# Kernel tuning notes

Measured on AMD Instinct MI355X. Metric: run time of the kernel, lower is better.

## Reference

```python
import jax, jax.numpy as jnp
import numpy as np

B, N, IN_DIM, D, H, L = 8, 256, 2, 128, 512, 2
EPS = 1e-5


def layer_norm(x, g, b):
    m = jnp.mean(x, axis=-1, keepdims=True)
    v = jnp.var(x, axis=-1, keepdims=True)
    return (x - m) * jax.lax.rsqrt(v + EPS) * g + b


def loo_max_pool(nodes):
    # nodes: (B, N, D) -> leave-one-out max over the set axis -> (B, N, D)
    n = nodes.shape[1]
    neg = jnp.finfo(nodes.dtype).min
    mask = jnp.eye(n, dtype=bool)[None, :, :, None]          # (1, N, N, 1)
    expanded = jnp.broadcast_to(nodes[:, None, :, :],
                                (nodes.shape[0], n, n, nodes.shape[2]))
    return jnp.where(mask, neg, expanded).max(axis=2)        # (B, N, D)


def setup_inputs() -> dict:
    key = jax.random.key(0)
    ks = jax.random.split(key, 16)
    s = 0.02
    inp = {
        "x":   jax.random.normal(ks[0], (B, N, IN_DIM), dtype=jnp.float32),
        # embedding linear + its LayerNorm
        "We":  jax.random.normal(ks[1], (IN_DIM, D)) * s,
        "be":  jnp.zeros((D,), jnp.float32),
        "ge":  jnp.ones((D,), jnp.float32),
        "bge": jnp.zeros((D,), jnp.float32),
        # per-layer pool linear (concat of x and LOO-pooled context: 2D -> D)
        "Wp":  jax.random.normal(ks[2], (L, 2 * D, D)) * s,
        "bp":  jnp.zeros((L, D), jnp.float32),
        "gp":  jnp.ones((L, D), jnp.float32),
        "bgp": jnp.zeros((L, D), jnp.float32),
        # per-layer feed-forward D -> H -> D
        "W1":  jax.random.normal(ks[3], (L, D, H)) * s,
        "b1":  jnp.zeros((L, H), jnp.float32),
        "W2":  jax.random.normal(ks[4], (L, H, D)) * s,
        "b2":  jnp.zeros((L, D), jnp.float32),
        "gf":  jnp.ones((L, D), jnp.float32),
        "bgf": jnp.zeros((L, D), jnp.float32),
    }
    return inp


def reference(x, We, be, ge, bge, Wp, bp, gp, bgp, W1, b1, W2, b2, gf, bgf):
    # embeddings + embedding norm
    h = layer_norm(x @ We + be, ge, bge)                      # (B, N, D)
    for i in range(L):
        # pool layer: LOO max pooling, concat, linear, residual, norm
        pooled = loo_max_pool(h)                              # (B, N, D)
        cat = jnp.concatenate([h, pooled], axis=-1)           # (B, N, 2D)
        h = layer_norm(h + cat @ Wp[i] + bp[i], gp[i], bgp[i])
        # feed-forward, residual, norm
        ff = jax.nn.relu(h @ W1[i] + b1[i]) @ W2[i] + b2[i]
        h = layer_norm(h + ff, gf[i], bgf[i])
    return h
```

## Files before the change

### kernel.cpp

```cpp
#include <hip/hip_runtime.h>
#include <hip/hip_bf16.h>

#define BB 8
#define NN 256
#define DD 128
#define HH 512
#define LL 2
#define EPSV 1e-5f
#define TPE 4
#define TPB 8
#define BPE (NN/TPE)
#define BPL (NN/TPB)
#define NEMB ((BB*NN)/TPE)

typedef unsigned short ushort_t;
typedef __attribute__((ext_vector_type(8))) short bf16x8;
typedef __attribute__((ext_vector_type(4))) float f32x4;

__device__ __forceinline__ ushort_t f2b(float v){
  __hip_bfloat16 h = __float2bfloat16(v);
  return *(ushort_t*)&h;
}

__device__ __forceinline__ void waveRed2(float &a, float &b){
  #pragma unroll
  for (int off=32; off>=1; off>>=1){
    a += __shfl_xor(a, off, 64);
    b += __shfl_xor(b, off, 64);
  }
}

__device__ __forceinline__ void poolMerge(float &m1, float &m2, int &am,
                                          float o1, float o2, int oa){
  if (o1 > m1){ m2 = fmaxf(m1, o2); m1 = o1; am = oa; }
  else        { m2 = fmaxf(m2, o1); }
}

__global__ __launch_bounds__(512) void k_prep(
    const float* __restrict__ x, const float* __restrict__ We,
    const float* __restrict__ be, const float* __restrict__ ge,
    const float* __restrict__ bge, float* __restrict__ h,
    float* __restrict__ pm1p, float* __restrict__ pm2p, int* __restrict__ pargp,
    const float* __restrict__ Wp, const float* __restrict__ W1,
    const float* __restrict__ W2, ushort_t* __restrict__ wpT,
    ushort_t* __restrict__ w1T, ushort_t* __restrict__ w2T)
{
  __shared__ float tile[32][33];
  __shared__ float red[TPE][2][2];
  __shared__ float hf[TPE][DD];

  if (blockIdx.x < NEMB){
    int tid = threadIdx.x;
    int t = tid >> 7, d = tid & 127;
    int lane = tid & 63, wid = (tid >> 6) & 1;
    int t0 = blockIdx.x * TPE;
    int tok = t0 + t;
    float x0 = x[tok*2], x1 = x[tok*2+1];
    float v = fmaf(x0, We[d], fmaf(x1, We[DD+d], be[d]));
    float s=v, q=v*v; waveRed2(s,q);
    if (lane==0){ red[t][wid][0]=s; red[t][wid][1]=q; }
    __syncthreads();
    float S=red[t][0][0]+red[t][1][0], Q=red[t][0][1]+red[t][1][1];
    float m=S*(1.f/DD), var=Q*(1.f/DD)-m*m, rs=rsqrtf(var+EPSV);
    float hv = (v-m)*rs*ge[d] + bge[d];
    h[(size_t)tok*DD + d] = hv;
    hf[t][d] = hv;
    __syncthreads();
    if (t==0){
      int b = t0 >> 8;
      int n0 = t0 & 255;
      float m1 = hf[0][d], m2 = -3.4e38f; int am = n0;
      #pragma unroll
      for (int p=1;p<TPE;++p) poolMerge(m1,m2,am, hf[p][d], -3.4e38f, n0+p);
      int blk = (t0 >> 2) & (BPE-1);
      size_t idx = ((size_t)b*BPE + blk)*DD + d;
      pm1p[idx]=m1; pm2p[idx]=m2; pargp[idx]=am;
    }
  } else {
    if (threadIdx.x >= 256) return;
    int bid = blockIdx.x - NEMB;
    const float* src; ushort_t* dst; int K, N, kt, nt;
    if (bid < 64){
      int l = bid >> 5, r = bid & 31;
      src = Wp + (size_t)l*256*128; dst = wpT + (size_t)l*128*256;
      K=256; N=128; kt = r >> 2; nt = r & 3;
    } else if (bid < 192){
      int e = bid - 64; int l = e >> 6, r = e & 63;
      src = W1 + (size_t)l*128*512; dst = w1T + (size_t)l*512*128;
      K=128; N=512; kt = r >> 4; nt = r & 15;
    } else {
      int e = bid - 192; int l = e >> 6, r = e & 63;
      src = W2 + (size_t)l*512*128; dst = w2T + (size_t)l*128*512;
      K=512; N=128; kt = r >> 2; nt = r & 3;
    }
    int k0 = kt*32, n0 = nt*32;
    int tx = threadIdx.x & 31, ty = threadIdx.x >> 5;
    #pragma unroll
    for (int i=0;i<4;++i)
      tile[ty + i*8][tx] = src[(size_t)(k0+ty+i*8)*N + n0 + tx];
    __syncthreads();
    #pragma unroll
    for (int i=0;i<4;++i)
      dst[(size_t)(n0+ty+i*8)*K + k0 + tx] = f2b(tile[tx][ty + i*8]);
  }
}

__global__ __launch_bounds__(512, 2) void k_layer(
    float* __restrict__ h,
    const float* __restrict__ pm1p, const float* __restrict__ pm2p,
    const int* __restrict__ pargp, int npart,
    float* __restrict__ qm1p, float* __restrict__ qm2p, int* __restrict__ qargp,
    int write_pool,
    const ushort_t* __restrict__ WpT, const float* __restrict__ bp,
    const float* __restrict__ gp, const float* __restrict__ bgp,
    const ushort_t* __restrict__ W1T, const float* __restrict__ b1,
    const ushort_t* __restrict__ W2T, const float* __restrict__ b2,
    const float* __restrict__ gf, const float* __restrict__ bgf)
{
  int tid = threadIdx.x;
  int d = tid & 127, fourth = tid >> 7;
  int wv = tid >> 6;
  int lane = tid & 63;
  int m = lane & 15, q = lane >> 4;
  int t0 = blockIdx.x * TPB;
  int b = t0 >> 8;

  __shared__ ushort_t catb[16*256];
  __shared__ float    hres[8*128];
  __shared__ float    sA[16*128];
  __shared__ ushort_t h1b[16*128];
  __shared__ float    h1f[8*128];
  __shared__ ushort_t ub[16*512];
  __shared__ float fm1[128], fm2[128];
  __shared__ int   fam[128];
  __shared__ float sm1[4][128], sm2[4][128];
  __shared__ int   sam[4][128];

  int n0a = wv*16;
  bf16x8 wfA[8];
  {
    const ushort_t* wp = WpT + (size_t)(n0a+m)*256 + q*8;
    #pragma unroll
    for (int ks=0; ks<8; ++ks) wfA[ks] = *(const bf16x8*)(wp + ks*32);
  }
  bf16x8 wfB[16];
  {
    #pragma unroll
    for (int i=0;i<4;++i){
      int n0 = i*128 + wv*16;
      const ushort_t* wp = W1T + (size_t)(n0+m)*128 + q*8;
      #pragma unroll
      for (int ks=0; ks<4; ++ks) wfB[i*4+ks] = *(const bf16x8*)(wp + ks*32);
    }
  }

  {
    int per = npart >> 2;
    size_t base = ((size_t)b*npart + fourth*per)*DD + d;
    float m1 = pm1p[base], m2 = pm2p[base]; int am = pargp[base];
    for (int i=1;i<per;++i)
      poolMerge(m1,m2,am, pm1p[base+(size_t)i*DD], pm2p[base+(size_t)i*DD],
                pargp[base+(size_t)i*DD]);
    sm1[fourth][d]=m1; sm2[fourth][d]=m2; sam[fourth][d]=am;
  }
  __syncthreads();
  if (fourth==0){
    float m1=sm1[0][d], m2=sm2[0][d]; int am=sam[0][d];
    #pragma unroll
    for (int p=1;p<4;++p) poolMerge(m1,m2,am, sm1[p][d], sm2[p][d], sam[p][d]);
    fm1[d]=m1; fm2[d]=m2; fam[d]=am;
  }
  __syncthreads();

  #pragma unroll
  for (int rep=0; rep<4; ++rep){
    int e = rep*512 + tid;
    int t = e >> 8, c = e & 255;
    int tok = t0 + t, n = (t0 & 255) + t;
    float v;
    if (c < DD){ v = h[(size_t)tok*DD + c]; hres[t*128 + c] = v; }
    else { int cc = c - DD; v = (n==fam[cc]) ? fm2[cc] : fm1[cc]; }
    catb[t*256 + c] = f2b(v);
  }
  __syncthreads();

  {
    f32x4 acc = {0.f,0.f,0.f,0.f};
    const ushort_t* ap = catb + m*256 + q*8;
    #pragma unroll
    for (int ks=0; ks<8; ++ks){
      bf16x8 af = *(const bf16x8*)(ap + ks*32);
      acc = __builtin_amdgcn_mfma_f32_16x16x32_bf16(af, wfA[ks], acc, 0,0,0);
    }
    #pragma unroll
    for (int r=0;r<4;++r) sA[(q*4+r)*128 + n0a + m] = acc[r];
  }

  bf16x8 wfC[16];
  {
    const ushort_t* wp = W2T + (size_t)(n0a+m)*512 + q*8;
    #pragma unroll
    for (int ks=0; ks<16; ++ks) wfC[ks] = *(const bf16x8*)(wp + ks*32);
  }
  __syncthreads();

  {
    int t = wv, g = lane;
    float2 v2 = *(const float2*)&sA[t*128 + 2*g];
    float v0 = v2.x + bp[2*g]   + hres[t*128 + 2*g];
    float v1 = v2.y + bp[2*g+1] + hres[t*128 + 2*g + 1];
    float s = v0+v1, qq = v0*v0 + v1*v1;
    waveRed2(s,qq);
    float mean = s*(1.f/128), var = qq*(1.f/128) - mean*mean;
    float rs = rsqrtf(var + EPSV);
    float o0 = (v0-mean)*rs*gp[2*g]   + bgp[2*g];
    float o1 = (v1-mean)*rs*gp[2*g+1] + bgp[2*g+1];
    unsigned pk = (unsigned)f2b(o0) | ((unsigned)f2b(o1) << 16);
    *(unsigned*)&h1b[t*128 + 2*g] = pk;
    *(float2*)&h1f[t*128 + 2*g] = make_float2(o0, o1);
  }
  __syncthreads();

  {
    const ushort_t* ap = h1b + m*128 + q*8;
    bf16x8 af[4];
    #pragma unroll
    for (int ks=0; ks<4; ++ks) af[ks] = *(const bf16x8*)(ap + ks*32);
    #pragma unroll
    for (int i=0;i<4;++i){
      int n0 = i*128 + wv*16;
      f32x4 acc = {0.f,0.f,0.f,0.f};
      #pragma unroll
      for (int ks=0; ks<4; ++ks)
        acc = __builtin_amdgcn_mfma_f32_16x16x32_bf16(af[ks], wfB[i*4+ks], acc, 0,0,0);
      float bb = b1[n0+m];
      #pragma unroll
      for (int r=0;r<4;++r)
        ub[(q*4+r)*512 + n0 + m] = f2b(fmaxf(acc[r] + bb, 0.f));
    }
  }
  __syncthreads();

  {
    f32x4 acc = {0.f,0.f,0.f,0.f};
    const ushort_t* ap = ub + m*512 + q*8;
    #pragma unroll
    for (int ks=0; ks<16; ++ks){
      bf16x8 af = *(const bf16x8*)(ap + ks*32);
      acc = __builtin_amdgcn_mfma_f32_16x16x32_bf16(af, wfC[ks], acc, 0,0,0);
    }
    #pragma unroll
    for (int r=0;r<4;++r) sA[(q*4+r)*128 + n0a + m] = acc[r];
  }
  __syncthreads();

  {
    int t = wv, g = lane;
    float2 v2 = *(const float2*)&sA[t*128 + 2*g];
    float v0 = v2.x + b2[2*g]   + h1f[t*128 + 2*g];
    float v1 = v2.y + b2[2*g+1] + h1f[t*128 + 2*g + 1];
    float s = v0+v1, qq = v0*v0 + v1*v1;
    waveRed2(s,qq);
    float mean = s*(1.f/128), var = qq*(1.f/128) - mean*mean;
    float rs = rsqrtf(var + EPSV);
    float o0 = (v0-mean)*rs*gf[2*g]   + bgf[2*g];
    float o1 = (v1-mean)*rs*gf[2*g+1] + bgf[2*g+1];
    *(float2*)&h[(size_t)(t0+t)*DD + 2*g] = make_float2(o0, o1);
    *(float2*)&hres[t*128 + 2*g] = make_float2(o0, o1);
  }
  if (write_pool){
    __syncthreads();
    if (tid < 128){
      int n0 = t0 & 255;
      float m1 = hres[tid], m2 = -3.4e38f; int am = n0;
      #pragma unroll
      for (int p=1;p<TPB;++p)
        poolMerge(m1,m2,am, hres[p*128 + tid], -3.4e38f, n0+p);
      int blk = (t0 >> 3) & (BPL-1);
      size_t idx = ((size_t)b*BPL + blk)*DD + tid;
      qm1p[idx]=m1; qm2p[idx]=m2; qargp[idx]=am;
    }
  }
}

extern "C" void kernel_launch(void* const* d_in, const int* in_sizes, int n_in,
                              void* d_out, int out_size, void* d_ws, size_t ws_size,
                              hipStream_t stream)
{
  const float* x   = (const float*)d_in[0];
  const float* We  = (const float*)d_in[1];
  const float* be  = (const float*)d_in[2];
  const float* ge  = (const float*)d_in[3];
  const float* bge = (const float*)d_in[4];
  const float* Wp  = (const float*)d_in[5];
  const float* bp  = (const float*)d_in[6];
  const float* gp  = (const float*)d_in[7];
  const float* bgp = (const float*)d_in[8];
  const float* W1  = (const float*)d_in[9];
  const float* b1  = (const float*)d_in[10];
  const float* W2  = (const float*)d_in[11];
  const float* b2  = (const float*)d_in[12];
  const float* gf  = (const float*)d_in[13];
  const float* bgf = (const float*)d_in[14];

  float* h = (float*)d_out;
  char* ws = (char*)d_ws;
  const size_t NA = (size_t)BB*BPE*DD;
  const size_t NB = (size_t)BB*BPL*DD;
  float* pA1 = (float*)ws;                    ws += NA*4;
  float* pA2 = (float*)ws;                    ws += NA*4;
  int*   pAa = (int*)ws;                      ws += NA*4;
  float* pB1 = (float*)ws;                    ws += NB*4;
  float* pB2 = (float*)ws;                    ws += NB*4;
  int*   pBa = (int*)ws;                      ws += NB*4;
  ushort_t* wpT = (ushort_t*)ws;              ws += (size_t)LL*DD*2*DD*2;
  ushort_t* w1T = (ushort_t*)ws;              ws += (size_t)LL*HH*DD*2;
  ushort_t* w2T = (ushort_t*)ws;              ws += (size_t)LL*DD*HH*2;

  k_prep<<<NEMB + 320, 512, 0, stream>>>(x, We, be, ge, bge, h,
      pA1, pA2, pAa, Wp, W1, W2, wpT, w1T, w2T);

  k_layer<<<(BB*NN)/TPB, 512, 0, stream>>>(h, pA1, pA2, pAa, BPE,
      pB1, pB2, pBa, 1,
      wpT,                     bp,       gp,       bgp,
      w1T,                     b1,       w2T,      b2,
      gf,                      bgf);

  k_layer<<<(BB*NN)/TPB, 512, 0, stream>>>(h, pB1, pB2, pBa, BPL,
      pB1, pB2, pBa, 0,
      wpT + (size_t)DD*2*DD,   bp + DD,  gp + DD,  bgp + DD,
      w1T + (size_t)HH*DD,     b1 + HH,  w2T + (size_t)DD*HH, b2 + DD,
      gf + DD,                 bgf + DD);
}
```

Measured before the change: 123.1 us.

## Fuse prep and both layers into one cooperative persistent kernel with grid syncs

Replaces the three launches (prep, layer 0, layer 1) with a single cooperative kernel of 256 blocks. Between stages it uses grid.sync, and each block's hidden state stays in shared memory across layers instead of going through global memory. The embedding, the pool partials and the weight transposes now run inside the same blocks. This removes launch gaps and global round-trips of h, at the cost of grid-wide barriers and a single large kernel whose register and LDS footprint must still allow all blocks to be co-resident.

After: 288.2 us. +134.1%, slower.

```diff
diff --git a/kernel.cpp b/kernel.cpp
--- a/kernel.cpp
+++ b/kernel.cpp
@@ -1,5 +1,6 @@
 #include <hip/hip_runtime.h>
 #include <hip/hip_bf16.h>
+#include <hip/hip_cooperative_groups.h>
 
 #define BB 8
 #define NN 256
@@ -7,11 +8,8 @@
 #define HH 512
 #define LL 2
 #define EPSV 1e-5f
-#define TPE 4
 #define TPB 8
-#define BPE (NN/TPE)
 #define BPL (NN/TPB)
-#define NEMB ((BB*NN)/TPE)
 
 typedef unsigned short ushort_t;
 typedef __attribute__((ext_vector_type(8))) short bf16x8;
@@ -36,87 +34,20 @@
   else        { m2 = fmaxf(m2, o1); }
 }
 
-__global__ __launch_bounds__(512) void k_prep(
-    const float* __restrict__ x, const float* __restrict__ We,
-    const float* __restrict__ be, const float* __restrict__ ge,
-    const float* __restrict__ bge, float* __restrict__ h,
-    float* __restrict__ pm1p, float* __restrict__ pm2p, int* __restrict__ pargp,
-    const float* __restrict__ Wp, const float* __restrict__ W1,
-    const float* __restrict__ W2, ushort_t* __restrict__ wpT,
-    ushort_t* __restrict__ w1T, ushort_t* __restrict__ w2T)
+struct KParams {
+  const float *x, *We, *be, *ge, *bge;
+  const float *Wp, *bp, *gp, *bgp;
+  const float *W1, *b1, *W2, *b2, *gf, *bgf;
+  float *h;
+  float *p01, *p02; int *p0a;
+  float *p11, *p12; int *p1a;
+  ushort_t *wpT, *w1T, *w2T;
+};
+
+__global__ __launch_bounds__(512, 2) void k_fused(KParams P)
 {
-  __shared__ float tile[32][33];
-  __shared__ float red[TPE][2][2];
-  __shared__ float hf[TPE][DD];
-
-  if (blockIdx.x < NEMB){
-    int tid = threadIdx.x;
-    int t = tid >> 7, d = tid & 127;
-    int lane = tid & 63, wid = (tid >> 6) & 1;
-    int t0 = blockIdx.x * TPE;
-    int tok = t0 + t;
-    float x0 = x[tok*2], x1 = x[tok*2+1];
-    float v = fmaf(x0, We[d], fmaf(x1, We[DD+d], be[d]));
-    float s=v, q=v*v; waveRed2(s,q);
-    if (lane==0){ red[t][wid][0]=s; red[t][wid][1]=q; }
-    __syncthreads();
-    float S=red[t][0][0]+red[t][1][0], Q=red[t][0][1]+red[t][1][1];
-    float m=S*(1.f/DD), var=Q*(1.f/DD)-m*m, rs=rsqrtf(var+EPSV);
-    float hv = (v-m)*rs*ge[d] + bge[d];
-    h[(size_t)tok*DD + d] = hv;
-    hf[t][d] = hv;
-    __syncthreads();
-    if (t==0){
-      int b = t0 >> 8;
-      int n0 = t0 & 255;
-      float m1 = hf[0][d], m2 = -3.4e38f; int am = n0;
-      #pragma unroll
-      for (int p=1;p<TPE;++p) poolMerge(m1,m2,am, hf[p][d], -3.4e38f, n0+p);
-      int blk = (t0 >> 2) & (BPE-1);
-      size_t idx = ((size_t)b*BPE + blk)*DD + d;
-      pm1p[idx]=m1; pm2p[idx]=m2; pargp[idx]=am;
-    }
-  } else {
-    if (threadIdx.x >= 256) return;
-    int bid = blockIdx.x - NEMB;
-    const float* src; ushort_t* dst; int K, N, kt, nt;
-    if (bid < 64){
-      int l = bid >> 5, r = bid & 31;
-      src = Wp + (size_t)l*256*128; dst = wpT + (size_t)l*128*256;
-      K=256; N=128; kt = r >> 2; nt = r & 3;
-    } else if (bid < 192){
-      int e = bid - 64; int l = e >> 6, r = e & 63;
-      src = W1 + (size_t)l*128*512; dst = w1T + (size_t)l*512*128;
-      K=128; N=512; kt = r >> 4; nt = r & 15;
-    } else {
-      int e = bid - 192; int l = e >> 6, r = e & 63;
-      src = W2 + (size_t)l*512*128; dst = w2T + (size_t)l*128*512;
-      K=512; N=128; kt = r >> 2; nt = r & 3;
-    }
-    int k0 = kt*32, n0 = nt*32;
-    int tx = threadIdx.x & 31, ty = threadIdx.x >> 5;
-    #pragma unroll
-    for (int i=0;i<4;++i)
-      tile[ty + i*8][tx] = src[(size_t)(k0+ty+i*8)*N + n0 + tx];
-    __syncthreads();
-    #pragma unroll
-    for (int i=0;i<4;++i)
-      dst[(size_t)(n0+ty+i*8)*K + k0 + tx] = f2b(tile[tx][ty + i*8]);
-  }
-}
-
-__global__ __launch_bounds__(512, 2) void k_layer(
-    float* __restrict__ h,
-    const float* __restrict__ pm1p, const float* __restrict__ pm2p,
-    const int* __restrict__ pargp, int npart,
-    float* __restrict__ qm1p, float* __restrict__ qm2p, int* __restrict__ qargp,
-    int write_pool,
-    const ushort_t* __restrict__ WpT, const float* __restrict__ bp,
-    const float* __restrict__ gp, const float* __restrict__ bgp,
-    const ushort_t* __restrict__ W1T, const float* __restrict__ b1,
-    const ushort_t* __restrict__ W2T, const float* __restrict__ b2,
-    const float* __restrict__ gf, const float* __restrict__ bgf)
-{
+  cooperative_groups::grid_group grid = cooperative_groups::this_grid();
+
   int tid = threadIdx.x;
   int d = tid & 127, fourth = tid >> 7;
   int wv = tid >> 6;
@@ -124,9 +55,10 @@
   int m = lane & 15, q = lane >> 4;
   int t0 = blockIdx.x * TPB;
   int b = t0 >> 8;
-
+  int blk = (t0 >> 3) & (BPL-1);
+
+  __shared__ float    hcur[8*128];
   __shared__ ushort_t catb[16*256];
-  __shared__ float    hres[8*128];
   __shared__ float    sA[16*128];
   __shared__ ushort_t h1b[16*128];
   __shared__ float    h1f[8*128];
@@ -135,150 +67,234 @@
   __shared__ int   fam[128];
   __shared__ float sm1[4][128], sm2[4][128];
   __shared__ int   sam[4][128];
-
-  int n0a = wv*16;
-  bf16x8 wfA[8];
+  __shared__ float tile[32][33];
+  __shared__ float red[8][2][2];
+
   {
-    const ushort_t* wp = WpT + (size_t)(n0a+m)*256 + q*8;
+    float vv[2];
     #pragma unroll
-    for (int ks=0; ks<8; ++ks) wfA[ks] = *(const bf16x8*)(wp + ks*32);
-  }
-  bf16x8 wfB[16];
-  {
+    for (int rep=0; rep<2; ++rep){
+      int t = rep*4 + fourth;
+      int tok = t0 + t;
+      float x0 = P.x[tok*2], x1 = P.x[tok*2+1];
+      float v = fmaf(x0, P.We[d], fmaf(x1, P.We[DD+d], P.be[d]));
+      vv[rep] = v;
+      float s=v, qq=v*v; waveRed2(s,qq);
+      if (lane==0){ red[t][(tid>>6)&1][0]=s; red[t][(tid>>6)&1][1]=qq; }
+    }
+    __syncthreads();
     #pragma unroll
-    for (int i=0;i<4;++i){
-      int n0 = i*128 + wv*16;
-      const ushort_t* wp = W1T + (size_t)(n0+m)*128 + q*8;
-      #pragma unroll
-      for (int ks=0; ks<4; ++ks) wfB[i*4+ks] = *(const bf16x8*)(wp + ks*32);
-    }
-  }
-
-  {
-    int per = npart >> 2;
-    size_t base = ((size_t)b*npart + fourth*per)*DD + d;
-    float m1 = pm1p[base], m2 = pm2p[base]; int am = pargp[base];
-    for (int i=1;i<per;++i)
-      poolMerge(m1,m2,am, pm1p[base+(size_t)i*DD], pm2p[base+(size_t)i*DD],
-                pargp[base+(size_t)i*DD]);
-    sm1[fourth][d]=m1; sm2[fourth][d]=m2; sam[fourth][d]=am;
+    for (int rep=0; rep<2; ++rep){
+      int t = rep*4 + fourth;
+      float S=red[t][0][0]+red[t][1][0], Q=red[t][0][1]+red[t][1][1];
+      float mean=S*(1.f/DD), var=Q*(1.f/DD)-mean*mean, rs=rsqrtf(var+EPSV);
+      hcur[t*128 + d] = (vv[rep]-mean)*rs*P.ge[d] + P.bge[d];
+    }
   }
   __syncthreads();
-  if (fourth==0){
-    float m1=sm1[0][d], m2=sm2[0][d]; int am=sam[0][d];
+  if (tid < 128){
+    int n0 = t0 & 255;
+    float m1 = hcur[tid], m2 = -3.4e38f; int am = n0;
     #pragma unroll
-    for (int p=1;p<4;++p) poolMerge(m1,m2,am, sm1[p][d], sm2[p][d], sam[p][d]);
-    fm1[d]=m1; fm2[d]=m2; fam[d]=am;
-  }
-  __syncthreads();
-
-  #pragma unroll
-  for (int rep=0; rep<4; ++rep){
-    int e = rep*512 + tid;
-    int t = e >> 8, c = e & 255;
-    int tok = t0 + t, n = (t0 & 255) + t;
-    float v;
-    if (c < DD){ v = h[(size_t)tok*DD + c]; hres[t*128 + c] = v; }
-    else { int cc = c - DD; v = (n==fam[cc]) ? fm2[cc] : fm1[cc]; }
-    catb[t*256 + c] = f2b(v);
-  }
-  __syncthreads();
-
-  {
-    f32x4 acc = {0.f,0.f,0.f,0.f};
-    const ushort_t* ap = catb + m*256 + q*8;
+    for (int p=1;p<TPB;++p) poolMerge(m1,m2,am, hcur[p*128+tid], -3.4e38f, n0+p);
+    size_t idx = ((size_t)b*BPL + blk)*128 + tid;
+    P.p01[idx]=m1; P.p02[idx]=m2; P.p0a[idx]=am;
+  }
+  for (int bid = blockIdx.x; bid < 320; bid += 256){
+    const float* src; ushort_t* dst; int K, N, kt, nt;
+    if (bid < 64){
+      int l = bid >> 5, r = bid & 31;
+      src = P.Wp + (size_t)l*256*128; dst = P.wpT + (size_t)l*128*256;
+      K=256; N=128; kt = r >> 2; nt = r & 3;
+    } else if (bid < 192){
+      int e = bid - 64; int l = e >> 6, r = e & 63;
+      src = P.W1 + (size_t)l*128*512; dst = P.w1T + (size_t)l*512*128;
+      K=128; N=512; kt = r >> 4; nt = r & 15;
+    } else {
+      int e = bid - 192; int l = e >> 6, r = e & 63;
+      src = P.W2 + (size_t)l*512*128; dst = P.w2T + (size_t)l*128*512;
+      K=512; N=128; kt = r >> 2; nt = r & 3;
+    }
+    int k0 = kt*32, n0 = nt*32;
+    int tx = tid & 31, ty = (tid >> 5) & 7;
+    __syncthreads();
+    if (tid < 256){
+      #pragma unroll
+      for (int i=0;i<4;++i)
+        tile[ty + i*8][tx] = src[(size_t)(k0+ty+i*8)*N + n0 + tx];
+    }
+    __syncthreads();
+    if (tid < 256){
+      #pragma unroll
+      for (int i=0;i<4;++i)
+        dst[(size_t)(n0+ty+i*8)*K + k0 + tx] = f2b(tile[tx][ty + i*8]);
+    }
+  }
+  __threadfence();
+  grid.sync();
+
+  #pragma unroll 1
+  for (int l=0; l<2; ++l){
+    const ushort_t* WpT = P.wpT + (size_t)l*128*256;
+    const ushort_t* W1T = P.w1T + (size_t)l*512*128;
+    const ushort_t* W2T = P.w2T + (size_t)l*128*512;
+    const float* bp  = P.bp  + l*DD;
+    const float* gp  = P.gp  + l*DD;
+    const float* bgp = P.bgp + l*DD;
+    const float* b1  = P.b1  + l*HH;
+    const float* b2  = P.b2  + l*DD;
+    const float* gf  = P.gf  + l*DD;
+    const float* bgf = P.bgf + l*DD;
+    const float* pm1 = l ? P.p11 : P.p01;
+    const float* pm2 = l ? P.p12 : P.p02;
+    const int*   pma = l ? P.p1a : P.p0a;
+
+    int n0a = wv*16;
+    bf16x8 wfA[8];
+    {
+      const ushort_t* wp = WpT + (size_t)(n0a+m)*256 + q*8;
+      #pragma unroll
+      for (int ks=0; ks<8; ++ks) wfA[ks] = *(const bf16x8*)(wp + ks*32);
+    }
+    bf16x8 wfB[16];
+    {
+      #pragma unroll
+      for (int i=0;i<4;++i){
+        int n0 = i*128 + wv*16;
+        const ushort_t* wp = W1T + (size_t)(n0+m)*128 + q*8;
+        #pragma unroll
+        for (int ks=0; ks<4; ++ks) wfB[i*4+ks] = *(const bf16x8*)(wp + ks*32);
+      }
+    }
+    bf16x8 wfC[16];
+    {
+      const ushort_t* wp = W2T + (size_t)(n0a+m)*512 + q*8;
+      #pragma unroll
+      for (int ks=0; ks<16; ++ks) wfC[ks] = *(const bf16x8*)(wp + ks*32);
+    }
+
+    {
+      size_t base = ((size_t)b*BPL + fourth*8)*128 + d;
+      float m1 = pm1[base], m2 = pm2[base]; int am = pma[base];
+      #pragma unroll
+      for (int i=1;i<8;++i)
+        poolMerge(m1,m2,am, pm1[base+(size_t)i*128], pm2[base+(size_t)i*128],
+                  pma[base+(size_t)i*128]);
+      sm1[fourth][d]=m1; sm2[fourth][d]=m2; sam[fourth][d]=am;
+    }
+    __syncthreads();
+    if (fourth==0){
+      float m1=sm1[0][d], m2=sm2[0][d]; int am=sam[0][d];
+      #pragma unroll
+      for (int p=1;p<4;++p) poolMerge(m1,m2,am, sm1[p][d], sm2[p][d], sam[p][d]);
+      fm1[d]=m1; fm2[d]=m2; fam[d]=am;
+    }
+    __syncthreads();
+
     #pragma unroll
-    for (int ks=0; ks<8; ++ks){
-      bf16x8 af = *(const bf16x8*)(ap + ks*32);
-      acc = __builtin_amdgcn_mfma_f32_16x16x32_bf16(af, wfA[ks], acc, 0,0,0);
-    }
-    #pragma unroll
-    for (int r=0;r<4;++r) sA[(q*4+r)*128 + n0a + m] = acc[r];
-  }
-
-  bf16x8 wfC[16];
-  {
-    const ushort_t* wp = W2T + (size_t)(n0a+m)*512 + q*8;
-    #pragma unroll
-    for (int ks=0; ks<16; ++ks) wfC[ks] = *(const bf16x8*)(wp + ks*32);
-  }
-  __syncthreads();
-
-  {
-    int t = wv, g = lane;
-    float2 v2 = *(const float2*)&sA[t*128 + 2*g];
-    float v0 = v2.x + bp[2*g]   + hres[t*128 + 2*g];
-    float v1 = v2.y + bp[2*g+1] + hres[t*128 + 2*g + 1];
-    float s = v0+v1, qq = v0*v0 + v1*v1;
-    waveRed2(s,qq);
-    float mean = s*(1.f/128), var = qq*(1.f/128) - mean*mean;
-    float rs = rsqrtf(var + EPSV);
-    float o0 = (v0-mean)*rs*gp[2*g]   + bgp[2*g];
-    float o1 = (v1-mean)*rs*gp[2*g+1] + bgp[2*g+1];
-    unsigned pk = (unsigned)f2b(o0) | ((unsigned)f2b(o1) << 16);
-    *(unsigned*)&h1b[t*128 + 2*g] = pk;
-    *(float2*)&h1f[t*128 + 2*g] = make_float2(o0, o1);
-  }
-  __syncthreads();
-
-  {
-    const ushort_t* ap = h1b + m*128 + q*8;
-    bf16x8 af[4];
-    #pragma unroll
-    for (int ks=0; ks<4; ++ks) af[ks] = *(const bf16x8*)(ap + ks*32);
-    #pragma unroll
-    for (int i=0;i<4;++i){
-      int n0 = i*128 + wv*16;
+    for (int rep=0; rep<4; ++rep){
+      int e = rep*512 + tid;
+      int t = e >> 8, c = e & 255;
+      int n = (t0 & 255) + t;
+      float v;
+      if (c < DD) v = hcur[t*128 + c];
+      else { int cc = c - DD; v = (n==fam[cc]) ? fm2[cc] : fm1[cc]; }
+      catb[t*256 + c] = f2b(v);
+    }
+    __syncthreads();
+
+    {
       f32x4 acc = {0.f,0.f,0.f,0.f};
-      #pragma unroll
-      for (int ks=0; ks<4; ++ks)
-        acc = __builtin_amdgcn_mfma_f32_16x16x32_bf16(af[ks], wfB[i*4+ks], acc, 0,0,0);
-      float bb = b1[n0+m];
-      #pragma unroll
-      for (int r=0;r<4;++r)
-        ub[(q*4+r)*512 + n0 + m] = f2b(fmaxf(acc[r] + bb, 0.f));
-    }
-  }
-  __syncthreads();
-
-  {
-    f32x4 acc = {0.f,0.f,0.f,0.f};
-    const ushort_t* ap = ub + m*512 + q*8;
-    #pragma unroll
-    for (int ks=0; ks<16; ++ks){
-      bf16x8 af = *(const bf16x8*)(ap + ks*32);
-      acc = __builtin_amdgcn_mfma_f32_16x16x32_bf16(af, wfC[ks], acc, 0,0,0);
-    }
-    #pragma unroll
-    for (int r=0;r<4;++r) sA[(q*4+r)*128 + n0a + m] = acc[r];
-  }
-  __syncthreads();
-
-  {
-    int t = wv, g = lane;
-    float2 v2 = *(const float2*)&sA[t*128 + 2*g];
-    float v0 = v2.x + b2[2*g]   + h1f[t*128 + 2*g];
-    float v1 = v2.y + b2[2*g+1] + h1f[t*128 + 2*g + 1];
-    float s = v0+v1, qq = v0*v0 + v1*v1;
-    waveRed2(s,qq);
-    float mean = s*(1.f/128), var = qq*(1.f/128) - mean*mean;
-    float rs = rsqrtf(var + EPSV);
-    float o0 = (v0-mean)*rs*gf[2*g]   + bgf[2*g];
-    float o1 = (v1-mean)*rs*gf[2*g+1] + bgf[2*g+1];
-    *(float2*)&h[(size_t)(t0+t)*DD + 2*g] = make_float2(o0, o1);
-    *(float2*)&hres[t*128 + 2*g] = make_float2(o0, o1);
-  }
-  if (write_pool){
-    __syncthreads();
-    if (tid < 128){
-      int n0 = t0 & 255;
-      float m1 = hres[tid], m2 = -3.4e38f; int am = n0;
-      #pragma unroll
-      for (int p=1;p<TPB;++p)
-        poolMerge(m1,m2,am, hres[p*128 + tid], -3.4e38f, n0+p);
-      int blk = (t0 >> 3) & (BPL-1);
-      size_t idx = ((size_t)b*BPL + blk)*DD + tid;
-      qm1p[idx]=m1; qm2p[idx]=m2; qargp[idx]=am;
+      const ushort_t* ap = catb + m*256 + q*8;
+      #pragma unroll
+      for (int ks=0; ks<8; ++ks){
+        bf16x8 af = *(const bf16x8*)(ap + ks*32);
+        acc = __builtin_amdgcn_mfma_f32_16x16x32_bf16(af, wfA[ks], acc, 0,0,0);
+      }
+      #pragma unroll
+      for (int r=0;r<4;++r) sA[(q*4+r)*128 + n0a + m] = acc[r];
+    }
+    __syncthreads();
+
+    {
+      int t = wv, g = lane;
+      float2 v2 = *(const float2*)&sA[t*128 + 2*g];
+      float v0 = v2.x + bp[2*g]   + hcur[t*128 + 2*g];
+      float v1 = v2.y + bp[2*g+1] + hcur[t*128 + 2*g + 1];
+      float s = v0+v1, qq = v0*v0 + v1*v1;
+      waveRed2(s,qq);
+      float mean = s*(1.f/128), var = qq*(1.f/128) - mean*mean;
+      float rs = rsqrtf(var + EPSV);
+      float o0 = (v0-mean)*rs*gp[2*g]   + bgp[2*g];
+      float o1 = (v1-mean)*rs*gp[2*g+1] + bgp[2*g+1];
+      unsigned pk = (unsigned)f2b(o0) | ((unsigned)f2b(o1) << 16);
+      *(unsigned*)&h1b[t*128 + 2*g] = pk;
+      *(float2*)&h1f[t*128 + 2*g] = make_float2(o0, o1);
+    }
+    __syncthreads();
+
+    {
+      const ushort_t* ap = h1b + m*128 + q*8;
+      bf16x8 af[4];
+      #pragma unroll
+      for (int ks=0; ks<4; ++ks) af[ks] = *(const bf16x8*)(ap + ks*32);
+      #pragma unroll
+      for (int i=0;i<4;++i){
+        int n0 = i*128 + wv*16;
+        f32x4 acc = {0.f,0.f,0.f,0.f};
+        #pragma unroll
+        for (int ks=0; ks<4; ++ks)
+          acc = __builtin_amdgcn_mfma_f32_16x16x32_bf16(af[ks], wfB[i*4+ks], acc, 0,0,0);
+        float bb = b1[n0+m];
+        #pragma unroll
+        for (int r=0;r<4;++r)
+          ub[(q*4+r)*512 + n0 + m] = f2b(fmaxf(acc[r] + bb, 0.f));
+      }
+    }
+    __syncthreads();
+
+    {
+      f32x4 acc = {0.f,0.f,0.f,0.f};
+      const ushort_t* ap = ub + m*512 + q*8;
+      #pragma unroll
+      for (int ks=0; ks<16; ++ks){
+        bf16x8 af = *(const bf16x8*)(ap + ks*32);
+        acc = __builtin_amdgcn_mfma_f32_16x16x32_bf16(af, wfC[ks], acc, 0,0,0);
+      }
+      #pragma unroll
+      for (int r=0;r<4;++r) sA[(q*4+r)*128 + n0a + m] = acc[r];
+    }
+    __syncthreads();
+
+    {
+      int t = wv, g = lane;
+      float2 v2 = *(const float2*)&sA[t*128 + 2*g];
+      float v0 = v2.x + b2[2*g]   + h1f[t*128 + 2*g];
+      float v1 = v2.y + b2[2*g+1] + h1f[t*128 + 2*g + 1];
+      float s = v0+v1, qq = v0*v0 + v1*v1;
+      waveRed2(s,qq);
+      float mean = s*(1.f/128), var = qq*(1.f/128) - mean*mean;
+      float rs = rsqrtf(var + EPSV);
+      float o0 = (v0-mean)*rs*gf[2*g]   + bgf[2*g];
+      float o1 = (v1-mean)*rs*gf[2*g+1] + bgf[2*g+1];
+      *(float2*)&hcur[t*128 + 2*g] = make_float2(o0, o1);
+      if (l == LL-1)
+        *(float2*)&P.h[(size_t)(t0+t)*DD + 2*g] = make_float2(o0, o1);
+    }
+
+    if (l == 0){
+      __syncthreads();
+      if (tid < 128){
+        int n0 = t0 & 255;
+        float m1 = hcur[tid], m2 = -3.4e38f; int am = n0;
+        #pragma unroll
+        for (int p=1;p<TPB;++p)
+          poolMerge(m1,m2,am, hcur[p*128+tid], -3.4e38f, n0+p);
+        size_t idx = ((size_t)b*BPL + blk)*128 + tid;
+        P.p11[idx]=m1; P.p12[idx]=m2; P.p1a[idx]=am;
+      }
+      __threadfence();
+      grid.sync();
     }
   }
 }
@@ -287,48 +303,36 @@
                               void* d_out, int out_size, void* d_ws, size_t ws_size,
                               hipStream_t stream)
 {
-  const float* x   = (const float*)d_in[0];
-  const float* We  = (const float*)d_in[1];
-  const float* be  = (const float*)d_in[2];
-  const float* ge  = (const float*)d_in[3];
-  const float* bge = (const float*)d_in[4];
-  const float* Wp  = (const float*)d_in[5];
-  const float* bp  = (const float*)d_in[6];
-  const float* gp  = (const float*)d_in[7];
-  const float* bgp = (const float*)d_in[8];
-  const float* W1  = (const float*)d_in[9];
-  const float* b1  = (const float*)d_in[10];
-  const float* W2  = (const float*)d_in[11];
-  const float* b2  = (const float*)d_in[12];
-  const float* gf  = (const float*)d_in[13];
-  const float* bgf = (const float*)d_in[14];
-
-  float* h = (float*)d_out;
   char* ws = (char*)d_ws;
-  const size_t NA = (size_t)BB*BPE*DD;
-  const size_t NB = (size_t)BB*BPL*DD;
-  float* pA1 = (float*)ws;                    ws += NA*4;
-  float* pA2 = (float*)ws;                    ws += NA*4;
-  int*   pAa = (int*)ws;                      ws += NA*4;
-  float* pB1 = (float*)ws;                    ws += NB*4;
-  float* pB2 = (float*)ws;                    ws += NB*4;
-  int*   pBa = (int*)ws;                      ws += NB*4;
-  ushort_t* wpT = (ushort_t*)ws;              ws += (size_t)LL*DD*2*DD*2;
-  ushort_t* w1T = (ushort_t*)ws;              ws += (size_t)LL*HH*DD*2;
-  ushort_t* w2T = (ushort_t*)ws;              ws += (size_t)LL*DD*HH*2;
-
-  k_prep<<<NEMB + 320, 512, 0, stream>>>(x, We, be, ge, bge, h,
-      pA1, pA2, pAa, Wp, W1, W2, wpT, w1T, w2T);
-
-  k_layer<<<(BB*NN)/TPB, 512, 0, stream>>>(h, pA1, pA2, pAa, BPE,
-      pB1, pB2, pBa, 1,
-      wpT,                     bp,       gp,       bgp,
-      w1T,                     b1,       w2T,      b2,
-      gf,                      bgf);
-
-  k_layer<<<(BB*NN)/TPB, 512, 0, stream>>>(h, pB1, pB2, pBa, BPL,
-      pB1, pB2, pBa, 0,
-      wpT + (size_t)DD*2*DD,   bp + DD,  gp + DD,  bgp + DD,
-      w1T + (size_t)HH*DD,     b1 + HH,  w2T + (size_t)DD*HH, b2 + DD,
-      gf + DD,                 bgf + DD);
-}
+  const size_t NP = (size_t)BB*BPL*128;
+  KParams P;
+  P.x   = (const float*)d_in[0];
+  P.We  = (const float*)d_in[1];
+  P.be  = (const float*)d_in[2];
+  P.ge  = (const float*)d_in[3];
+  P.bge = (const float*)d_in[4];
+  P.Wp  = (const float*)d_in[5];
+  P.bp  = (const float*)d_in[6];
+  P.gp  = (const float*)d_in[7];
+  P.bgp = (const float*)d_in[8];
+  P.W1  = (const float*)d_in[9];
+  P.b1  = (const float*)d_in[10];
+  P.W2  = (const float*)d_in[11];
+  P.b2  = (const float*)d_in[12];
+  P.gf  = (const float*)d_in[13];
+  P.bgf = (const float*)d_in[14];
+  P.h   = (float*)d_out;
+  P.p01 = (float*)ws;                ws += NP*4;
+  P.p02 = (float*)ws;                ws += NP*4;
+  P.p0a = (int*)ws;                  ws += NP*4;
+  P.p11 = (float*)ws;                ws += NP*4;
+  P.p12 = (float*)ws;                ws += NP*4;
+  P.p1a = (int*)ws;                  ws += NP*4;
+  P.wpT = (ushort_t*)ws;             ws += (size_t)LL*128*256*2;
+  P.w1T = (ushort_t*)ws;             ws += (size_t)LL*512*128*2;
+  P.w2T = (ushort_t*)ws;             ws += (size_t)LL*128*512*2;
+
+  void* args[] = { (void*)&P };
+  hipLaunchCooperativeKernel(reinterpret_cast<void*>(k_fused),
+                             dim3((BB*NN)/TPB), dim3(512), args, 0, stream);
+}
```
